# Performance work log

Hardware: AMD Instinct MI355X
Metric: run time of the kernel (lower is better)

## Reference

```python
import jax, jax.numpy as jnp
import numpy as np

D_MODEL = 256
EXPAND = 2
MAX_STEPS = 6
DILATIONS = (1, 2, 4)
EPS = 1e-6


def setup_inputs() -> dict:
    key = jax.random.key(0)
    ks = jax.random.split(key, 12)
    B, C, H, W = 8, D_MODEL, 64, 64
    d, dh = D_MODEL, D_MODEL * EXPAND
    init_logit = float(np.log(0.1 / (0.25 - 0.1 + 1e-08)))
    s = 1.0 / np.sqrt(d)
    return {
        "u": jax.random.normal(ks[0], (B, C, H, W), jnp.float32),
        "forcing": jax.random.normal(ks[1], (B, C, H, W), jnp.float32),
        "diff_logits": jnp.full((3, d), init_logit, jnp.float32),
        "w1": jax.random.uniform(ks[2], (d, dh), jnp.float32, -s, s),
        "b1": jax.random.uniform(ks[3], (dh,), jnp.float32, -s, s),
        "w2": jax.random.uniform(ks[4], (dh, d), jnp.float32, -1.0 / np.sqrt(dh), 1.0 / np.sqrt(dh)),
        "b2": jax.random.uniform(ks[5], (d,), jnp.float32, -1.0 / np.sqrt(dh), 1.0 / np.sqrt(dh)),
        "wf": jax.random.uniform(ks[6], (d, d), jnp.float32, -s, s),
        "bf": jax.random.uniform(ks[7], (d,), jnp.float32, -s, s),
        "wi": jax.random.uniform(ks[8], (d, d), jnp.float32, -s, s),
        "bi": jax.random.uniform(ks[9], (d,), jnp.float32, -s, s),
        "wc": jax.random.uniform(ks[10], (d, d), jnp.float32, -s, s),
        "bc": jax.random.uniform(ks[11], (d,), jnp.float32, -s, s),
        "norm_scale": jnp.ones((d,), jnp.float32),
        "log_dt": jnp.asarray(np.log(0.1), jnp.float32),
        "alpha_mem": jnp.asarray(0.1, jnp.float32),
        "alpha_force": jnp.asarray(0.1, jnp.float32),
    }


def _laplacian(u, diff_logits):
    # multi-dilation 5-point reflect-padded stencil, per-channel coeffs
    out = jnp.zeros_like(u)
    for i, d in enumerate(DILATIONS):
        coeff = 0.25 * jax.nn.sigmoid(diff_logits[i])  # (C,)
        p = jnp.pad(u, ((0, 0), (0, 0), (d, d), (d, d)), mode="reflect")
        lap = (p[:, :, d:-d, 2 * d:] + p[:, :, d:-d, :-2 * d]
               + p[:, :, 2 * d:, d:-d] + p[:, :, :-2 * d, d:-d] - 4.0 * u)
        out = out + coeff[None, :, None, None] * lap
    return out


def reference(u, forcing, diff_logits, w1, b1, w2, b2, wf, bf, wi, bi, wc, bc,
              norm_scale, log_dt, alpha_mem, alpha_force):
    B, C, H, W = u.shape
    dt = jnp.clip(jnp.exp(log_dt), 0.01, 0.3)
    h = jnp.zeros((B, C), u.dtype)
    inv_sqrt_c = 1.0 / float(np.sqrt(C))
    for t in range(MAX_STEPS):
        diff = _laplacian(u, diff_logits)
        # per-cell reaction MLP on channel axis (exact GELU, matching torch)
        hdn = jax.nn.gelu(jnp.einsum("bchw,ce->behw", u, w1) + b1[None, :, None, None],
                          approximate=False)
        react = jnp.einsum("behw,ec->bchw", hdn, w2) + b2[None, :, None, None]
        # gated global memory on pooled features
        pooled = u.mean(axis=(2, 3))  # (B, C)
        f = jax.nn.sigmoid(pooled @ wf + bf)
        i_ = jax.nn.sigmoid(pooled @ wi + bi)
        c = jnp.tanh(pooled @ wc + bc)
        h = h * f + i_ * c
        du = diff + react + alpha_mem * h[:, :, None, None] + alpha_force * forcing
        u = u + dt * du
        if (t + 1) % 2 == 0:
            # RMSNorm over channel dim
            rms = jnp.sqrt(jnp.sum(u * u, axis=1, keepdims=True)) * inv_sqrt_c
            u = u / (rms + EPS) * norm_scale[None, :, None, None]
    return u
```

## Files before the change

kernel.cpp:

```cpp
#include <hip/hip_runtime.h>
#include <math.h>

constexpr int NB = 8, NC = 256, NE = 512, NH = 64, NW = 64, NHW = NH * NW;
constexpr int STEPS = 6;

typedef short bfrag8 __attribute__((ext_vector_type(8)));
typedef float f32x4 __attribute__((ext_vector_type(4)));

__device__ __forceinline__ float sigm_(float x) { return 1.f / (1.f + expf(-x)); }
__device__ __forceinline__ float gelu_(float x) {
    return 0.5f * x * (1.f + erff(x * 0.70710678118654752f));
}
__device__ __forceinline__ ushort f2bf(float f) {
    unsigned u = __builtin_bit_cast(unsigned, f);
    unsigned r = (u + 0x7fffu + ((u >> 16) & 1u)) >> 16;
    return (ushort)r;
}
__device__ __forceinline__ float bf2f(ushort us) {
    return __builtin_bit_cast(float, (unsigned)us << 16);
}
__device__ __forceinline__ void gload16(const void* g, void* l) {
    __builtin_amdgcn_global_load_lds((const __attribute__((address_space(1))) void*)g,
                                     (__attribute__((address_space(3))) void*)l, 16, 0, 0);
}

__global__ void wt_kernel(const float* __restrict__ w1, const float* __restrict__ w2,
                          ushort* __restrict__ w1t, ushort* __restrict__ w2t) {
    const int bid = blockIdx.x, tid = threadIdx.x;
    if (bid < NE) {
        w1t[bid * NC + tid] = f2bf(w1[(size_t)tid * NE + bid]);
    } else {
        const int c = bid - NE;
        for (int e = tid; e < NE; e += 256)
            w2t[c * NE + e] = f2bf(w2[(size_t)e * NC + c]);
    }
}

__global__ void fconv_kernel(const float* __restrict__ fin, ushort* __restrict__ fout) {
    const size_t i8 = ((size_t)blockIdx.x * 256 + threadIdx.x) * 8;
    const float4 a = *reinterpret_cast<const float4*>(fin + i8);
    const float4 b = *reinterpret_cast<const float4*>(fin + i8 + 4);
    uint4 o;
    o.x = (unsigned)f2bf(a.x) | ((unsigned)f2bf(a.y) << 16);
    o.y = (unsigned)f2bf(a.z) | ((unsigned)f2bf(a.w) << 16);
    o.z = (unsigned)f2bf(b.x) | ((unsigned)f2bf(b.y) << 16);
    o.w = (unsigned)f2bf(b.z) | ((unsigned)f2bf(b.w) << 16);
    *reinterpret_cast<uint4*>(fout + i8) = o;
}

__global__ __launch_bounds__(256) void x0_kernel(const float* __restrict__ u,
                                                 ushort* __restrict__ X,
                                                 float* __restrict__ rowsums) {
    __shared__ ushort xs[64][264];
    const int tid = threadIdx.x;
    const int b = blockIdx.x >> 6, y = blockIdx.x & 63;
    const float* up = u + (size_t)b * NC * NHW + y * NW;
#pragma unroll
    for (int cc = 0; cc < 4; ++cc)
#pragma unroll
        for (int i = 0; i < 16; ++i) {
            const int idx = i * 256 + tid;
            const int c = idx >> 6, x = idx & 63;
            xs[x][cc * 64 + c] = f2bf(up[(size_t)(cc * 64 + c) * NHW + x]);
        }
    __syncthreads();
    ushort* Xp = X + ((size_t)b * NHW + y * NW) * NC;
    const int wv = tid >> 6, lane = tid & 63;
#pragma unroll
    for (int r = 0; r < 16; ++r) {
        const int row = wv * 16 + r;
        *reinterpret_cast<uint2*>(Xp + (size_t)row * NC + lane * 4) =
            *reinterpret_cast<const uint2*>(&xs[row][lane * 4]);
    }
    const float* rp = up + (size_t)tid * NHW;
    float s = 0.f;
#pragma unroll
    for (int x = 0; x < 64; ++x) s += rp[x];
    rowsums[((size_t)b * 64 + y) * NC + tid] = s;
}

__global__ __launch_bounds__(768) void gates_kernel(
    const float* __restrict__ rowsums,
    const float* __restrict__ wf, const float* __restrict__ bfv,
    const float* __restrict__ wi, const float* __restrict__ biv,
    const float* __restrict__ wc, const float* __restrict__ bcv,
    float* __restrict__ h, const int first) {
    const int b = blockIdx.x;
    const int tid = threadIdx.x;
    const int g = tid >> 8, c = tid & 255;
    __shared__ float sp[256];
    __shared__ float psum[3][256];
    __shared__ float gf[256], gi[256];
    const int y0 = (g == 0) ? 0 : (g == 1) ? 21 : 42;
    const int y1 = (g == 0) ? 21 : (g == 1) ? 42 : 64;
    const float* rs = rowsums + (size_t)b * 64 * NC + c;
    float s = 0.f;
    for (int y = y0; y < y1; ++y) s += rs[y * NC];
    psum[g][c] = s;
    __syncthreads();
    if (g == 0) sp[c] = (psum[0][c] + psum[1][c] + psum[2][c]) * (1.f / 4096.f);
    __syncthreads();
    const float* W  = (g == 0) ? wf  : (g == 1) ? wi  : wc;
    const float* Bv = (g == 0) ? bfv : (g == 1) ? biv : bcv;
    float a = Bv[c];
#pragma unroll 8
    for (int k = 0; k < 256; ++k) a = fmaf(sp[k], W[k * NC + c], a);
    if (g == 0) gf[c] = sigm_(a);
    else if (g == 1) gi[c] = sigm_(a);
    __syncthreads();
    if (g == 2) {
        const float cc = tanhf(a);
        const float hold = first ? 0.f : h[b * NC + c];
        h[b * NC + c] = hold * gf[c] + gi[c] * cc;
    }
}

__global__ __launch_bounds__(512, 4) void step_kernel(
    const ushort* __restrict__ Xg, const ushort* __restrict__ w1t,
    const ushort* __restrict__ w2t, const float* __restrict__ b1,
    const float* __restrict__ b2, const float* __restrict__ uin,
    const ushort* __restrict__ forc, const float* __restrict__ dlog,
    const float* __restrict__ hbuf, const float* __restrict__ nsc,
    const float* __restrict__ p_logdt, const float* __restrict__ p_am,
    const float* __restrict__ p_af, const int do_norm,
    float* __restrict__ uout, ushort* __restrict__ Xout,
    float* __restrict__ rowsums) {
    __shared__ __align__(16) char pool[73728];
    ushort* Xs = (ushort*)pool;
    ushort* Wb = (ushort*)(pool + 32768);
    ushort* Hs = (ushort*)(pool + 65536);

    const int tid = threadIdx.x;
    const int wv = tid >> 6, lane = tid & 63;
    const int r16 = lane & 15, kg = lane >> 4;
    const int work = (blockIdx.x & 7) * 64 + (blockIdx.x >> 3);
    const int b = work >> 6, y = work & 63;
    const int m0 = work * 64;

#pragma unroll
    for (int i = 0; i < 4; ++i) {
        const int idx = i * 512 + tid, row = idx >> 5, s = idx & 31;
        gload16(Xg + (size_t)(m0 + row) * NC + ((s ^ (row & 7)) << 3), Xs + idx * 8);
    }

    f32x4 acc2[2][4];
#pragma unroll
    for (int ct = 0; ct < 2; ++ct)
#pragma unroll
        for (int p = 0; p < 4; ++p) acc2[ct][p] = (f32x4){0.f, 0.f, 0.f, 0.f};

    const int epart = wv >> 1, pxh = wv & 1;

    for (int ec = 0; ec < 8; ++ec) {
        __syncthreads();
#pragma unroll
        for (int i = 0; i < 4; ++i) {
            const int idx = i * 512 + tid, row = idx >> 5, s = idx & 31;
            gload16(w1t + (size_t)(ec * 64 + row) * NC + ((s ^ (row & 7)) << 3),
                    Wb + idx * 8);
        }
        __syncthreads();
        f32x4 acc1[2];
#pragma unroll
        for (int p = 0; p < 2; ++p) acc1[p] = (f32x4){0.f, 0.f, 0.f, 0.f};
#pragma unroll
        for (int kk = 0; kk < 8; ++kk) {
            const int g = kk * 4 + kg;
            const int rowA = epart * 16 + r16;
            const bfrag8 a = *(const bfrag8*)(Wb + rowA * 256 + ((g ^ (rowA & 7)) << 3));
#pragma unroll
            for (int p = 0; p < 2; ++p) {
                const int rowB = pxh * 32 + p * 16 + r16;
                const bfrag8 bb = *(const bfrag8*)(Xs + rowB * 256 + ((g ^ (rowB & 7)) << 3));
                acc1[p] = __builtin_amdgcn_mfma_f32_16x16x32_bf16(a, bb, acc1[p], 0, 0, 0);
            }
        }
        __syncthreads();
        const float4 b1v = *(const float4*)(b1 + ec * 64 + epart * 16 + kg * 4);
        const float bj[4] = {b1v.x, b1v.y, b1v.z, b1v.w};
#pragma unroll
        for (int p = 0; p < 2; ++p) {
            ushort4 hv;
            hv.x = f2bf(gelu_(acc1[p][0] + bj[0]));
            hv.y = f2bf(gelu_(acc1[p][1] + bj[1]));
            hv.z = f2bf(gelu_(acc1[p][2] + bj[2]));
            hv.w = f2bf(gelu_(acc1[p][3] + bj[3]));
            const int px = pxh * 32 + p * 16 + r16;
            const int gr = epart * 2 + (kg >> 1);
            *(ushort4*)(Hs + px * 64 + ((gr ^ (px & 7)) << 3) + ((kg & 1) << 2)) = hv;
        }
#pragma unroll
        for (int i = 0; i < 4; ++i) {
            const int idx = i * 512 + tid, row = idx >> 3, s = idx & 7;
            gload16(w2t + (size_t)row * NE + ec * 64 + ((s ^ (row & 7)) << 3),
                    Wb + idx * 8);
        }
        __syncthreads();
#pragma unroll
        for (int kk = 0; kk < 2; ++kk) {
            const int g = kk * 4 + kg;
            bfrag8 bfr[4];
#pragma unroll
            for (int p = 0; p < 4; ++p) {
                const int rowB = p * 16 + r16;
                bfr[p] = *(const bfrag8*)(Hs + rowB * 64 + ((g ^ (rowB & 7)) << 3));
            }
#pragma unroll
            for (int ct = 0; ct < 2; ++ct) {
                const int rowA = wv * 32 + ct * 16 + r16;
                const bfrag8 a = *(const bfrag8*)(Wb + rowA * 64 + ((g ^ (rowA & 7)) << 3));
#pragma unroll
                for (int p = 0; p < 4; ++p)
                    acc2[ct][p] = __builtin_amdgcn_mfma_f32_16x16x32_bf16(a, bfr[p],
                                                                          acc2[ct][p], 0, 0, 0);
            }
        }
    }

    float* trh = (float*)pool;
    float* su  = (float*)(pool + 34816);
    const int eg2 = tid >> 4, pg = tid & 15, x0p = pg * 4;
    const float dt = fminf(fmaxf(expf(p_logdt[0]), 0.01f), 0.3f);
    const float am = p_am[0], afc = p_af[0];
    const float* ub = uin + (size_t)b * NC * NHW;
    const ushort* frow = forc + (size_t)b * NC * NHW + (size_t)y * NW;

    float unew[2][4][4];

#pragma unroll
    for (int h2 = 0; h2 < 2; ++h2) {
        __syncthreads();
        if ((wv >> 2) == h2) {
#pragma unroll
            for (int ct = 0; ct < 2; ++ct)
#pragma unroll
                for (int p = 0; p < 4; ++p)
#pragma unroll
                    for (int j = 0; j < 4; ++j)
                        trh[((wv & 3) * 32 + ct * 16 + kg * 4 + j) * 68 + p * 16 + r16] =
                            acc2[ct][p][j];
        }
#pragma unroll
        for (int i = 0; i < 4; ++i) {
            const int idx = i * 512 + tid;
            const int r = idx >> 4, q = (idx & 15) * 4;
            *(float4*)&su[r * 68 + q] =
                *(const float4*)(ub + (size_t)(h2 * 128 + r) * NHW + (size_t)y * NW + q);
        }
        __syncthreads();
#pragma unroll
        for (int jc = 0; jc < 4; ++jc) {
            const int crel = eg2 * 4 + jc;
            const int c = h2 * 128 + crel;
            const float co0 = 0.25f * sigm_(dlog[c]);
            const float co1 = 0.25f * sigm_(dlog[NC + c]);
            const float co2 = 0.25f * sigm_(dlog[2 * NC + c]);
            const float hterm = am * hbuf[b * NC + c];
            const float b2v = b2[c];
            const float* up = ub + (size_t)c * NHW;

            float ym[6][4];
            const int dy[6] = {-1, 1, -2, 2, -4, 4};
#pragma unroll
            for (int n = 0; n < 6; ++n) {
                int ry = y + dy[n];
                ry = ry < 0 ? -ry : (ry > 63 ? 126 - ry : ry);
                const float4 t = *reinterpret_cast<const float4*>(up + (size_t)ry * NW + x0p);
                ym[n][0] = t.x; ym[n][1] = t.y; ym[n][2] = t.z; ym[n][3] = t.w;
            }
            const uint2 fr = *reinterpret_cast<const uint2*>(frow + (size_t)c * NHW + x0p);
            float fv[4];
            fv[0] = bf2f((ushort)(fr.x & 0xffff));
            fv[1] = bf2f((ushort)(fr.x >> 16));
            fv[2] = bf2f((ushort)(fr.y & 0xffff));
            fv[3] = bf2f((ushort)(fr.y >> 16));
            const f32x4 rv = *reinterpret_cast<const f32x4*>(&trh[crel * 68 + x0p]);
#pragma unroll
            for (int ip = 0; ip < 4; ++ip) {
                const int x = x0p + ip;
                const float uc = su[crel * 68 + x];
                int xm, xp2;
                float dsum = 0.f, lap;
                xm = x - 1; xm = xm < 0 ? -xm : xm;
                xp2 = x + 1; xp2 = xp2 > 63 ? 126 - xp2 : xp2;
                lap = su[crel * 68 + xm] + su[crel * 68 + xp2] + ym[0][ip] + ym[1][ip] - 4.f * uc;
                dsum = fmaf(co0, lap, dsum);
                xm = x - 2; xm = xm < 0 ? -xm : xm;
                xp2 = x + 2; xp2 = xp2 > 63 ? 126 - xp2 : xp2;
                lap = su[crel * 68 + xm] + su[crel * 68 + xp2] + ym[2][ip] + ym[3][ip] - 4.f * uc;
                dsum = fmaf(co1, lap, dsum);
                xm = x - 4; xm = xm < 0 ? -xm : xm;
                xp2 = x + 4; xp2 = xp2 > 63 ? 126 - xp2 : xp2;
                lap = su[crel * 68 + xm] + su[crel * 68 + xp2] + ym[4][ip] + ym[5][ip] - 4.f * uc;
                dsum = fmaf(co2, lap, dsum);

                const float du_ = dsum + rv[ip] + b2v + hterm + afc * fv[ip];
                unew[h2][jc][ip] = uc + dt * du_;
            }
        }
    }
    __syncthreads();

    float* redc   = (float*)(pool + 34816);
    float* inv64p = (float*)(pool + 43520);
    if (do_norm) {
        float ps[4] = {0.f, 0.f, 0.f, 0.f};
#pragma unroll
        for (int h2 = 0; h2 < 2; ++h2)
#pragma unroll
            for (int jc = 0; jc < 4; ++jc)
#pragma unroll
                for (int ip = 0; ip < 4; ++ip)
                    ps[ip] = fmaf(unew[h2][jc][ip], unew[h2][jc][ip], ps[ip]);
        *reinterpret_cast<f32x4*>(&redc[eg2 * 68 + x0p]) = (f32x4){ps[0], ps[1], ps[2], ps[3]};
        __syncthreads();
        if (tid < 64) {
            float s = 0.f;
#pragma unroll
            for (int g = 0; g < 32; ++g) s += redc[g * 68 + tid];
            inv64p[tid] = 1.f / (sqrtf(s) * 0.0625f + 1e-6f);
        }
    }
    __syncthreads();

    ushort* xs = (ushort*)pool;
    float* sums = (float*)(pool + 52224);
    float persum[2][4];
    float* uob = uout + (size_t)b * NC * NHW + (size_t)y * NW;
#pragma unroll
    for (int h2 = 0; h2 < 2; ++h2) {
        float vsc[4][4];
#pragma unroll
        for (int jc = 0; jc < 4; ++jc) {
            const int c = h2 * 128 + eg2 * 4 + jc;
            const float ns = do_norm ? nsc[c] : 1.f;
#pragma unroll
            for (int ip = 0; ip < 4; ++ip) {
                float v = unew[h2][jc][ip];
                if (do_norm) v *= inv64p[x0p + ip] * ns;
                vsc[jc][ip] = v;
            }
            persum[h2][jc] = vsc[jc][0] + vsc[jc][1] + vsc[jc][2] + vsc[jc][3];
            float4 o; o.x = vsc[jc][0]; o.y = vsc[jc][1]; o.z = vsc[jc][2]; o.w = vsc[jc][3];
            *reinterpret_cast<float4*>(uob + (size_t)c * NHW + x0p) = o;
        }
#pragma unroll
        for (int ip = 0; ip < 4; ++ip) {
            ushort4 xv;
            xv.x = f2bf(vsc[0][ip]);
            xv.y = f2bf(vsc[1][ip]);
            xv.z = f2bf(vsc[2][ip]);
            xv.w = f2bf(vsc[3][ip]);
            *(ushort4*)(xs + (x0p + ip) * 270 + h2 * 128 + eg2 * 4) = xv;
        }
    }
#pragma unroll
    for (int h2 = 0; h2 < 2; ++h2)
#pragma unroll
        for (int jc = 0; jc < 4; ++jc)
            sums[(h2 * 128 + eg2 * 4 + jc) * 17 + pg] = persum[h2][jc];
    __syncthreads();
    ushort* Xp = Xout + (size_t)m0 * NC;
#pragma unroll
    for (int r = 0; r < 8; ++r) {
        const int row = wv * 8 + r;
        *reinterpret_cast<uint2*>(Xp + (size_t)row * NC + lane * 4) =
            *reinterpret_cast<const uint2*>(&xs[row * 270 + lane * 4]);
    }
    if (tid < 256) {
        float s = 0.f;
#pragma unroll
        for (int g = 0; g < 16; ++g) s += sums[tid * 17 + g];
        rowsums[((size_t)b * 64 + y) * NC + tid] = s;
    }
}

extern "C" void kernel_launch(void* const* d_in, const int* in_sizes, int n_in,
                              void* d_out, int out_size, void* d_ws, size_t ws_size,
                              hipStream_t stream) {
    (void)in_sizes; (void)n_in; (void)out_size; (void)ws_size;
    const float* u0      = (const float*)d_in[0];
    const float* forcing = (const float*)d_in[1];
    const float* dlog    = (const float*)d_in[2];
    const float* w1      = (const float*)d_in[3];
    const float* b1      = (const float*)d_in[4];
    const float* w2      = (const float*)d_in[5];
    const float* b2      = (const float*)d_in[6];
    const float* wf      = (const float*)d_in[7];
    const float* bfv     = (const float*)d_in[8];
    const float* wi      = (const float*)d_in[9];
    const float* biv     = (const float*)d_in[10];
    const float* wc      = (const float*)d_in[11];
    const float* bcv     = (const float*)d_in[12];
    const float* nsc     = (const float*)d_in[13];
    const float* p_logdt = (const float*)d_in[14];
    const float* p_am    = (const float*)d_in[15];
    const float* p_af    = (const float*)d_in[16];

    float* uout = (float*)d_out;

    char* w = (char*)d_ws;
    float*  uA     = (float*)w;   w += (size_t)NB * NC * NHW * 4;
    ushort* X      = (ushort*)w;  w += (size_t)NB * NHW * NC * 2;
    ushort* forc   = (ushort*)w;  w += (size_t)NB * NC * NHW * 2;
    ushort* w1t    = (ushort*)w;  w += (size_t)NE * NC * 2;
    ushort* w2t    = (ushort*)w;  w += (size_t)NC * NE * 2;
    float* rowsums = (float*)w;   w += (size_t)NB * NH * NC * 4;
    float* hbuf    = (float*)w;   w += (size_t)NB * NC * 4;

    wt_kernel<<<768, 256, 0, stream>>>(w1, w2, w1t, w2t);
    fconv_kernel<<<4096, 256, 0, stream>>>(forcing, forc);
    x0_kernel<<<NB * NH, 256, 0, stream>>>(u0, X, rowsums);

    const float* src = u0;
    for (int t = 0; t < STEPS; ++t) {
        float* dst = (t & 1) ? uout : uA;
        gates_kernel<<<NB, 768, 0, stream>>>(rowsums, wf, bfv, wi, biv, wc, bcv, hbuf, t == 0);
        step_kernel<<<NB * NH, 512, 0, stream>>>(X, w1t, w2t, b1, b2, src, forc, dlog,
                                                 hbuf, nsc, p_logdt, p_am, p_af,
                                                 ((t + 1) % 2) == 0, dst, X, rowsums);
        src = dst;
    }
}
```

Before: 590.6 us.

## Restructure MLP loop with 32-wide hidden chunks, prefetch and tanh GELU

The fused MLP loop in step_kernel now processes 16 chunks of 32 hidden units instead of 8 chunks of 64. It prefetches the next w1 tile while the second GEMM runs and double-buffers the hidden activations, cutting barriers per chunk. Exact erf GELU is replaced with a sigmoid-form tanh approximation using __expf. The diffusion sigmoid coefficients are precomputed once in wt_kernel, and the gate matvec uses four independent accumulators. The GELU approximation changes numerics slightly relative to the exact reference.

```diff
diff --git a/kernel.cpp b/kernel.cpp
--- a/kernel.cpp
+++ b/kernel.cpp
@@ -9,7 +9,8 @@
 
 __device__ __forceinline__ float sigm_(float x) { return 1.f / (1.f + expf(-x)); }
 __device__ __forceinline__ float gelu_(float x) {
-    return 0.5f * x * (1.f + erff(x * 0.70710678118654752f));
+    const float t2 = fmaf(0.0713548162f * x, x * x, 1.5957691216f * x);
+    return x / (1.f + __expf(-t2));
 }
 __device__ __forceinline__ ushort f2bf(float f) {
     unsigned u = __builtin_bit_cast(unsigned, f);
@@ -25,14 +26,20 @@
 }
 
 __global__ void wt_kernel(const float* __restrict__ w1, const float* __restrict__ w2,
-                          ushort* __restrict__ w1t, ushort* __restrict__ w2t) {
+                          const float* __restrict__ dlog,
+                          ushort* __restrict__ w1t, ushort* __restrict__ w2t,
+                          float* __restrict__ dcoef) {
     const int bid = blockIdx.x, tid = threadIdx.x;
     if (bid < NE) {
         w1t[bid * NC + tid] = f2bf(w1[(size_t)tid * NE + bid]);
-    } else {
+    } else if (bid < NE + NC) {
         const int c = bid - NE;
         for (int e = tid; e < NE; e += 256)
             w2t[c * NE + e] = f2bf(w2[(size_t)e * NC + c]);
+    } else {
+#pragma unroll
+        for (int i = 0; i < 3; ++i)
+            dcoef[i * NC + tid] = 0.25f * sigm_(dlog[i * NC + tid]);
     }
 }
 
@@ -102,9 +109,15 @@
     __syncthreads();
     const float* W  = (g == 0) ? wf  : (g == 1) ? wi  : wc;
     const float* Bv = (g == 0) ? bfv : (g == 1) ? biv : bcv;
-    float a = Bv[c];
-#pragma unroll 8
-    for (int k = 0; k < 256; ++k) a = fmaf(sp[k], W[k * NC + c], a);
+    float aA = 0.f, aB = 0.f, aC = 0.f, aD = 0.f;
+#pragma unroll 4
+    for (int k = 0; k < 256; k += 4) {
+        aA = fmaf(sp[k],     W[(size_t)(k)     * NC + c], aA);
+        aB = fmaf(sp[k + 1], W[(size_t)(k + 1) * NC + c], aB);
+        aC = fmaf(sp[k + 2], W[(size_t)(k + 2) * NC + c], aC);
+        aD = fmaf(sp[k + 3], W[(size_t)(k + 3) * NC + c], aD);
+    }
+    const float a = ((aA + aB) + (aC + aD)) + Bv[c];
     if (g == 0) gf[c] = sigm_(a);
     else if (g == 1) gi[c] = sigm_(a);
     __syncthreads();
@@ -119,16 +132,17 @@
     const ushort* __restrict__ Xg, const ushort* __restrict__ w1t,
     const ushort* __restrict__ w2t, const float* __restrict__ b1,
     const float* __restrict__ b2, const float* __restrict__ uin,
-    const ushort* __restrict__ forc, const float* __restrict__ dlog,
+    const ushort* __restrict__ forc, const float* __restrict__ dcoef,
     const float* __restrict__ hbuf, const float* __restrict__ nsc,
     const float* __restrict__ p_logdt, const float* __restrict__ p_am,
     const float* __restrict__ p_af, const int do_norm,
     float* __restrict__ uout, ushort* __restrict__ Xout,
     float* __restrict__ rowsums) {
-    __shared__ __align__(16) char pool[73728];
-    ushort* Xs = (ushort*)pool;
-    ushort* Wb = (ushort*)(pool + 32768);
-    ushort* Hs = (ushort*)(pool + 65536);
+    __shared__ __align__(16) char pool[75776];
+    ushort* Xs  = (ushort*)pool;
+    ushort* WAu = (ushort*)(pool + 32768);
+    ushort* WBu = (ushort*)(pool + 49152);
+    ushort* Hsu = (ushort*)(pool + 65536);
 
     const int tid = threadIdx.x;
     const int wv = tid >> 6, lane = tid & 63;
@@ -142,6 +156,11 @@
         const int idx = i * 512 + tid, row = idx >> 5, s = idx & 31;
         gload16(Xg + (size_t)(m0 + row) * NC + ((s ^ (row & 7)) << 3), Xs + idx * 8);
     }
+#pragma unroll
+    for (int i = 0; i < 2; ++i) {
+        const int idx = i * 512 + tid, row = idx >> 5, s = idx & 31;
+        gload16(w1t + (size_t)row * NC + ((s ^ (row & 7)) << 3), WAu + idx * 8);
+    }
 
     f32x4 acc2[2][4];
 #pragma unroll
@@ -149,72 +168,56 @@
 #pragma unroll
         for (int p = 0; p < 4; ++p) acc2[ct][p] = (f32x4){0.f, 0.f, 0.f, 0.f};
 
-    const int epart = wv >> 1, pxh = wv & 1;
-
-    for (int ec = 0; ec < 8; ++ec) {
-        __syncthreads();
-#pragma unroll
-        for (int i = 0; i < 4; ++i) {
-            const int idx = i * 512 + tid, row = idx >> 5, s = idx & 31;
-            gload16(w1t + (size_t)(ec * 64 + row) * NC + ((s ^ (row & 7)) << 3),
-                    Wb + idx * 8);
-        }
-        __syncthreads();
-        f32x4 acc1[2];
-#pragma unroll
-        for (int p = 0; p < 2; ++p) acc1[p] = (f32x4){0.f, 0.f, 0.f, 0.f};
+    const int eh = wv >> 2, pq = wv & 3;
+    __syncthreads();
+
+    for (int ec = 0; ec < 16; ++ec) {
+#pragma unroll
+        for (int i = 0; i < 2; ++i) {
+            const int idx = i * 512 + tid, row = idx >> 2, s = idx & 3;
+            const int sc = (s ^ ((row >> 1) & 3)) << 3;
+            gload16(w2t + (size_t)row * NE + ec * 32 + sc, WBu + idx * 8);
+        }
+        f32x4 acc1 = (f32x4){0.f, 0.f, 0.f, 0.f};
+        const int rA = eh * 16 + r16, rB = pq * 16 + r16;
 #pragma unroll
         for (int kk = 0; kk < 8; ++kk) {
             const int g = kk * 4 + kg;
-            const int rowA = epart * 16 + r16;
-            const bfrag8 a = *(const bfrag8*)(Wb + rowA * 256 + ((g ^ (rowA & 7)) << 3));
-#pragma unroll
-            for (int p = 0; p < 2; ++p) {
-                const int rowB = pxh * 32 + p * 16 + r16;
-                const bfrag8 bb = *(const bfrag8*)(Xs + rowB * 256 + ((g ^ (rowB & 7)) << 3));
-                acc1[p] = __builtin_amdgcn_mfma_f32_16x16x32_bf16(a, bb, acc1[p], 0, 0, 0);
+            const bfrag8 a = *(const bfrag8*)(WAu + rA * 256 + ((g ^ (rA & 7)) << 3));
+            const bfrag8 bb = *(const bfrag8*)(Xs + rB * 256 + ((g ^ (rB & 7)) << 3));
+            acc1 = __builtin_amdgcn_mfma_f32_16x16x32_bf16(a, bb, acc1, 0, 0, 0);
+        }
+        ushort* Hc = Hsu + (ec & 1) * 2560;
+        {
+            const int el = eh * 16 + kg * 4;
+            const float4 b1v = *(const float4*)(b1 + ec * 32 + el);
+            ushort4 hv;
+            hv.x = f2bf(gelu_(acc1[0] + b1v.x));
+            hv.y = f2bf(gelu_(acc1[1] + b1v.y));
+            hv.z = f2bf(gelu_(acc1[2] + b1v.z));
+            hv.w = f2bf(gelu_(acc1[3] + b1v.w));
+            *(ushort4*)(Hc + (pq * 16 + r16) * 40 + el) = hv;
+        }
+        __syncthreads();
+        if (ec < 15) {
+#pragma unroll
+            for (int i = 0; i < 2; ++i) {
+                const int idx = i * 512 + tid, row = idx >> 5, s = idx & 31;
+                gload16(w1t + (size_t)((ec + 1) * 32 + row) * NC + ((s ^ (row & 7)) << 3),
+                        WAu + idx * 8);
             }
         }
+#pragma unroll
+        for (int ct = 0; ct < 2; ++ct) {
+            const int rowA = wv * 32 + ct * 16 + r16;
+            const bfrag8 a2 = *(const bfrag8*)(WBu + rowA * 32 + ((kg ^ ((rowA >> 1) & 3)) << 3));
+#pragma unroll
+            for (int p = 0; p < 4; ++p) {
+                const bfrag8 bf2 = *(const bfrag8*)(Hc + (p * 16 + r16) * 40 + kg * 8);
+                acc2[ct][p] = __builtin_amdgcn_mfma_f32_16x16x32_bf16(a2, bf2, acc2[ct][p], 0, 0, 0);
+            }
+        }
         __syncthreads();
-        const float4 b1v = *(const float4*)(b1 + ec * 64 + epart * 16 + kg * 4);
-        const float bj[4] = {b1v.x, b1v.y, b1v.z, b1v.w};
-#pragma unroll
-        for (int p = 0; p < 2; ++p) {
-            ushort4 hv;
-            hv.x = f2bf(gelu_(acc1[p][0] + bj[0]));
-            hv.y = f2bf(gelu_(acc1[p][1] + bj[1]));
-            hv.z = f2bf(gelu_(acc1[p][2] + bj[2]));
-            hv.w = f2bf(gelu_(acc1[p][3] + bj[3]));
-            const int px = pxh * 32 + p * 16 + r16;
-            const int gr = epart * 2 + (kg >> 1);
-            *(ushort4*)(Hs + px * 64 + ((gr ^ (px & 7)) << 3) + ((kg & 1) << 2)) = hv;
-        }
-#pragma unroll
-        for (int i = 0; i < 4; ++i) {
-            const int idx = i * 512 + tid, row = idx >> 3, s = idx & 7;
-            gload16(w2t + (size_t)row * NE + ec * 64 + ((s ^ (row & 7)) << 3),
-                    Wb + idx * 8);
-        }
-        __syncthreads();
-#pragma unroll
-        for (int kk = 0; kk < 2; ++kk) {
-            const int g = kk * 4 + kg;
-            bfrag8 bfr[4];
-#pragma unroll
-            for (int p = 0; p < 4; ++p) {
-                const int rowB = p * 16 + r16;
-                bfr[p] = *(const bfrag8*)(Hs + rowB * 64 + ((g ^ (rowB & 7)) << 3));
-            }
-#pragma unroll
-            for (int ct = 0; ct < 2; ++ct) {
-                const int rowA = wv * 32 + ct * 16 + r16;
-                const bfrag8 a = *(const bfrag8*)(Wb + rowA * 64 + ((g ^ (rowA & 7)) << 3));
-#pragma unroll
-                for (int p = 0; p < 4; ++p)
-                    acc2[ct][p] = __builtin_amdgcn_mfma_f32_16x16x32_bf16(a, bfr[p],
-                                                                          acc2[ct][p], 0, 0, 0);
-            }
-        }
     }
 
     float* trh = (float*)pool;
@@ -252,9 +255,9 @@
         for (int jc = 0; jc < 4; ++jc) {
             const int crel = eg2 * 4 + jc;
             const int c = h2 * 128 + crel;
-            const float co0 = 0.25f * sigm_(dlog[c]);
-            const float co1 = 0.25f * sigm_(dlog[NC + c]);
-            const float co2 = 0.25f * sigm_(dlog[2 * NC + c]);
+            const float co0 = dcoef[c];
+            const float co1 = dcoef[NC + c];
+            const float co2 = dcoef[2 * NC + c];
             const float hterm = am * hbuf[b * NC + c];
             const float b2v = b2[c];
             const float* up = ub + (size_t)c * NHW;
@@ -407,8 +410,9 @@
     ushort* w2t    = (ushort*)w;  w += (size_t)NC * NE * 2;
     float* rowsums = (float*)w;   w += (size_t)NB * NH * NC * 4;
     float* hbuf    = (float*)w;   w += (size_t)NB * NC * 4;
-
-    wt_kernel<<<768, 256, 0, stream>>>(w1, w2, w1t, w2t);
+    float* dcoef   = (float*)w;   w += (size_t)3 * NC * 4;
+
+    wt_kernel<<<769, 256, 0, stream>>>(w1, w2, dlog, w1t, w2t, dcoef);
     fconv_kernel<<<4096, 256, 0, stream>>>(forcing, forc);
     x0_kernel<<<NB * NH, 256, 0, stream>>>(u0, X, rowsums);
 
@@ -416,7 +420,7 @@
     for (int t = 0; t < STEPS; ++t) {
         float* dst = (t & 1) ? uout : uA;
         gates_kernel<<<NB, 768, 0, stream>>>(rowsums, wf, bfv, wi, biv, wc, bcv, hbuf, t == 0);
-        step_kernel<<<NB * NH, 512, 0, stream>>>(X, w1t, w2t, b1, b2, src, forc, dlog,
+        step_kernel<<<NB * NH, 512, 0, stream>>>(X, w1t, w2t, b1, b2, src, forc, dcoef,
                                                  hbuf, nsc, p_logdt, p_am, p_af,
                                                  ((t + 1) % 2) == 0, dst, X, rowsums);
         src = dst;
```

After: 576.5 us. 2.4% less time.
